# Performance work log

Hardware: AMD Instinct MI355X
Metric: run time of the kernel (lower is better)

Reference implementation:

```python
import jax, jax.numpy as jnp
import numpy as np

DIM = 1024
D_SRC = 1024
H = 16
HD = DIM // H
SCALE = 1.0 / np.sqrt(DIM)  # module uses 1/sqrt(internal_dim), not head_dim


def setup_inputs() -> dict:
    key = jax.random.key(0)
    ks = jax.random.split(key, 7)
    B, T = 2, 2048
    Q = jax.random.normal(ks[0], (B, T, DIM), dtype=jnp.float32)
    K = jax.random.normal(ks[1], (B, T, D_SRC), dtype=jnp.float32)
    V = jax.random.normal(ks[2], (B, T, D_SRC), dtype=jnp.float32)
    # torch nn.Linear weights: (out_features, in_features); y = x @ W.T
    s = 0.02
    Wq = jax.random.normal(ks[3], (DIM, DIM), dtype=jnp.float32) * s
    Wk = jax.random.normal(ks[4], (DIM, D_SRC), dtype=jnp.float32) * s
    Wv = jax.random.normal(ks[5], (DIM, D_SRC), dtype=jnp.float32) * s
    Wo = jax.random.normal(ks[6], (DIM, DIM), dtype=jnp.float32) * s
    return {"Q": Q, "K": K, "V": V, "Wq": Wq, "Wk": Wk, "Wv": Wv, "Wo": Wo}


def _split_heads(x):  # (B,T,DIM) -> (B,H,T,HD)
    B, T, _ = x.shape
    return x.reshape(B, T, H, HD).transpose(0, 2, 1, 3)


def reference(Q, K, V, Wq, Wk, Wv, Wo):
    B, T, _ = Q.shape
    q = _split_heads(Q @ Wq.T)
    k = _split_heads(K @ Wk.T)
    v = _split_heads(V @ Wv.T)
    att = jnp.einsum('bhid,bhjd->bhij', q, k) * SCALE
    causal = jnp.tril(jnp.ones((T, T), dtype=bool))
    att = jnp.where(causal[None, None], att, -jnp.inf)
    att = jax.nn.softmax(att, axis=-1)
    y = jnp.einsum('bhij,bhjd->bhid', att, v)
    y = y.transpose(0, 2, 1, 3).reshape(B, T, DIM)
    y = y @ Wo.T
    return y, att
```

## Files before the change

### kernel.cpp

```cpp
#include <hip/hip_runtime.h>
#include <hip/hip_bf16.h>

#define Bb 2
#define Tt 2048
#define DIMd 1024
#define Hh 16
#define HDh 64
#define MTOK (Bb * Tt)
#define NSCALE 0.03125f

typedef __attribute__((ext_vector_type(8))) short bf16x8;
typedef __attribute__((ext_vector_type(4))) float floatx4;

__device__ __forceinline__ unsigned short f2bf(float f) {
    union { float f; unsigned int u; } a; a.f = f;
    const unsigned int u = a.u;
    return (unsigned short)((u + 0x7FFFu + ((u >> 16) & 1u)) >> 16);
}

__device__ __forceinline__ bf16x8 cvt8(const float4 a, const float4 b) {
    bf16x8 r;
    r[0] = (short)f2bf(a.x); r[1] = (short)f2bf(a.y);
    r[2] = (short)f2bf(a.z); r[3] = (short)f2bf(a.w);
    r[4] = (short)f2bf(b.x); r[5] = (short)f2bf(b.y);
    r[6] = (short)f2bf(b.z); r[7] = (short)f2bf(b.w);
    return r;
}

__device__ __forceinline__ void gl_lds16(const void* g, void* l) {
    __builtin_amdgcn_global_load_lds((const __attribute__((address_space(1))) void*)g,
                                     (__attribute__((address_space(3))) void*)l, 16, 0, 0);
}

__global__ __launch_bounds__(256) void f32_to_bf16(const float* __restrict__ src,
                                                   unsigned short* __restrict__ dst, int n) {
    const int i = (blockIdx.x * 256 + threadIdx.x) * 4;
    if (i < n) {
        const float4 v = *(const float4*)(src + i);
        ushort4 o;
        o.x = f2bf(v.x); o.y = f2bf(v.y); o.z = f2bf(v.z); o.w = f2bf(v.w);
        *(ushort4*)(dst + i) = o;
    }
}

__global__ __launch_bounds__(256) void gemm_bt_mfma(const unsigned short* __restrict__ A,
                                                    const unsigned short* __restrict__ W,
                                                    float* __restrict__ C,
                                                    int M, int N, int K) {
    __shared__ unsigned short As[128 * 32];
    __shared__ unsigned short Bs[128 * 32];

    const int tid  = threadIdx.x;
    const int wave = tid >> 6;
    const int lane = tid & 63;
    const int m0 = blockIdx.y * 128;
    const int n0 = blockIdx.x * 128;
    const int wm = (wave >> 1) * 64;
    const int wn = (wave & 1) * 64;
    const int qd = lane >> 4;
    const int ln16 = lane & 15;

    floatx4 acc[4][4];
#pragma unroll
    for (int mi = 0; mi < 4; ++mi)
#pragma unroll
        for (int ni = 0; ni < 4; ++ni) acc[mi][ni] = (floatx4){0.f, 0.f, 0.f, 0.f};

    for (int k0 = 0; k0 < K; k0 += 32) {
#pragma unroll
        for (int t = 0; t < 2; ++t) {
            const int c = t * 256 + wave * 64 + lane;
            const int row = c >> 2;
            const int col = (c & 3) * 8;
            gl_lds16(A + (size_t)(m0 + row) * K + k0 + col, &As[c * 8]);
            gl_lds16(W + (size_t)(n0 + row) * K + k0 + col, &Bs[c * 8]);
        }
        __syncthreads();

        bf16x8 af[4], bfr[4];
#pragma unroll
        for (int mi = 0; mi < 4; ++mi)
            af[mi] = *(const bf16x8*)&As[(wm + mi * 16 + ln16) * 32 + qd * 8];
#pragma unroll
        for (int ni = 0; ni < 4; ++ni)
            bfr[ni] = *(const bf16x8*)&Bs[(wn + ni * 16 + ln16) * 32 + qd * 8];
#pragma unroll
        for (int mi = 0; mi < 4; ++mi)
#pragma unroll
            for (int ni = 0; ni < 4; ++ni)
                acc[mi][ni] = __builtin_amdgcn_mfma_f32_16x16x32_bf16(af[mi], bfr[ni], acc[mi][ni], 0, 0, 0);
        __syncthreads();
    }

#pragma unroll
    for (int mi = 0; mi < 4; ++mi)
#pragma unroll
        for (int ni = 0; ni < 4; ++ni) {
            const int gn = n0 + wn + ni * 16 + ln16;
#pragma unroll
            for (int r = 0; r < 4; ++r) {
                const int gm = m0 + wm + mi * 16 + qd * 4 + r;
                C[(size_t)gm * N + gn] = acc[mi][ni][r];
            }
        }
}

#define PSTR 72

__global__ __launch_bounds__(256) void fused_attn(const float* __restrict__ qp,
                                                  const float* __restrict__ kp,
                                                  const float* __restrict__ vt,
                                                  float* __restrict__ att,
                                                  unsigned short* __restrict__ ymid,
                                                  float* __restrict__ lws) {
    __shared__ unsigned short Ks[64 * PSTR];
    __shared__ unsigned short Vs[64 * PSTR];
    __shared__ unsigned short Ps[64 * PSTR];
    __shared__ float ls[64];

    const int bid = blockIdx.x;
    const int bh  = bid & 31;
    const int it  = 31 - (bid >> 5);
    const int h   = bh & (Hh - 1);
    const int b   = bh >> 4;
    const int tid = threadIdx.x;
    const int w    = tid >> 6;
    const int lane = tid & 63;
    const int qd   = lane >> 4;
    const int ln16 = lane & 15;
    const int i0   = it * 64;

    if (tid < 64) ls[tid] = 0.f;

    bf16x8 qf[2];
    {
        const float* qrow = qp + (size_t)(b * Tt + i0 + w * 16 + ln16) * DIMd + h * HDh;
#pragma unroll
        for (int ks = 0; ks < 2; ++ks) {
            const float4 a = *(const float4*)(qrow + ks * 32 + qd * 8);
            const float4 c = *(const float4*)(qrow + ks * 32 + qd * 8 + 4);
            qf[ks] = cvt8(a, c);
        }
    }

    const int srow = tid >> 2;
    const int scol = (tid & 3) * 16;

    floatx4 oacc[4];
#pragma unroll
    for (int dt = 0; dt < 4; ++dt) oacc[dt] = (floatx4){0.f, 0.f, 0.f, 0.f};

    unsigned short* Pw = &Ps[w * 16 * PSTR];
    const int qrow0 = w * 16 + qd * 4;

    for (int jt = 0; jt <= it; ++jt) {
        const int j0 = jt * 64;
        __syncthreads();

        {
            const float* kr = kp + (size_t)(b * Tt + j0 + srow) * DIMd + h * HDh + scol;
            const float4 k0 = ((const float4*)kr)[0];
            const float4 k1 = ((const float4*)kr)[1];
            const float4 k2 = ((const float4*)kr)[2];
            const float4 k3 = ((const float4*)kr)[3];
            *(bf16x8*)&Ks[srow * PSTR + scol]     = cvt8(k0, k1);
            *(bf16x8*)&Ks[srow * PSTR + scol + 8] = cvt8(k2, k3);
            const float* vr = vt + (size_t)(h * HDh + srow) * MTOK + b * Tt + j0 + scol;
            const float4 v0 = ((const float4*)vr)[0];
            const float4 v1 = ((const float4*)vr)[1];
            const float4 v2 = ((const float4*)vr)[2];
            const float4 v3 = ((const float4*)vr)[3];
            *(bf16x8*)&Vs[srow * PSTR + scol]     = cvt8(v0, v1);
            *(bf16x8*)&Vs[srow * PSTR + scol + 8] = cvt8(v2, v3);
        }
        __syncthreads();

        floatx4 sacc[4];
#pragma unroll
        for (int ct = 0; ct < 4; ++ct) sacc[ct] = (floatx4){0.f, 0.f, 0.f, 0.f};
#pragma unroll
        for (int ks = 0; ks < 2; ++ks)
#pragma unroll
            for (int ct = 0; ct < 4; ++ct) {
                const bf16x8 kf = *(const bf16x8*)&Ks[(ct * 16 + ln16) * PSTR + ks * 32 + qd * 8];
                sacc[ct] = __builtin_amdgcn_mfma_f32_16x16x32_bf16(qf[ks], kf, sacc[ct], 0, 0, 0);
            }

        float rs[4] = {0.f, 0.f, 0.f, 0.f};
#pragma unroll
        for (int r = 0; r < 4; ++r) {
            const int ig = i0 + qrow0 + r;
            float* arow = att + (size_t)(bh * Tt + ig) * Tt + j0;
            unsigned short* prow = &Pw[(qd * 4 + r) * PSTR];
#pragma unroll
            for (int ct = 0; ct < 4; ++ct) {
                const int jc = ct * 16 + ln16;
                const float e = (j0 + jc <= ig) ? __expf(sacc[ct][r] * NSCALE) : 0.f;
                arow[jc] = e;
                prow[jc] = f2bf(e);
                rs[r] += e;
            }
        }
#pragma unroll
        for (int r = 0; r < 4; ++r) {
            float v = rs[r];
            v += __shfl_xor(v, 1); v += __shfl_xor(v, 2);
            v += __shfl_xor(v, 4); v += __shfl_xor(v, 8);
            if (ln16 == 0) ls[qrow0 + r] += v;
        }

#pragma unroll
        for (int ks = 0; ks < 2; ++ks) {
            const bf16x8 pf = *(const bf16x8*)&Pw[ln16 * PSTR + ks * 32 + qd * 8];
#pragma unroll
            for (int dt = 0; dt < 4; ++dt) {
                const bf16x8 vf = *(const bf16x8*)&Vs[(dt * 16 + ln16) * PSTR + ks * 32 + qd * 8];
                oacc[dt] = __builtin_amdgcn_mfma_f32_16x16x32_bf16(pf, vf, oacc[dt], 0, 0, 0);
            }
        }
    }

#pragma unroll
    for (int r = 0; r < 4; ++r) {
        const float inv = 1.f / ls[qrow0 + r];
        unsigned short* yr = ymid + (size_t)(b * Tt + i0 + qrow0 + r) * DIMd + h * HDh + ln16;
#pragma unroll
        for (int dt = 0; dt < 4; ++dt)
            yr[dt * 16] = f2bf(oacc[dt][r] * inv);
    }
    if (tid < 64) lws[bh * Tt + i0 + tid] = ls[tid];
}

__global__ __launch_bounds__(256) void att_rescale(float* __restrict__ att,
                                                   const float* __restrict__ lws) {
    const int row = blockIdx.x;
    const int i   = row & (Tt - 1);
    const float inv = 1.f / lws[row];
    float4* arow = (float4*)(att + (size_t)row * Tt);
    const int tid = threadIdx.x;
#pragma unroll
    for (int q = 0; q < 2; ++q) {
        const int f4 = tid + q * 256;
        const int j  = f4 * 4;
        float4 v;
        if (j <= i) {
            v = arow[f4];
            v.x = (j + 0 <= i) ? v.x * inv : 0.f;
            v.y = (j + 1 <= i) ? v.y * inv : 0.f;
            v.z = (j + 2 <= i) ? v.z * inv : 0.f;
            v.w = (j + 3 <= i) ? v.w * inv : 0.f;
        } else {
            v = make_float4(0.f, 0.f, 0.f, 0.f);
        }
        arow[f4] = v;
    }
}

extern "C" void kernel_launch(void* const* d_in, const int* in_sizes, int n_in,
                              void* d_out, int out_size, void* d_ws, size_t ws_size,
                              hipStream_t stream) {
    const float* Q  = (const float*)d_in[0];
    const float* K  = (const float*)d_in[1];
    const float* V  = (const float*)d_in[2];
    const float* Wq = (const float*)d_in[3];
    const float* Wk = (const float*)d_in[4];
    const float* Wv = (const float*)d_in[5];
    const float* Wo = (const float*)d_in[6];

    const size_t nytok = (size_t)Bb * Tt * DIMd;
    const size_t nw    = (size_t)DIMd * DIMd;
    float* y   = (float*)d_out;
    float* att = y + nytok;

    char* w = (char*)d_ws;
    float* qp = (float*)w;                       w += nytok * 4;
    float* kp = (float*)w;                       w += nytok * 4;
    float* vt = (float*)w;                       w += nytok * 4;
    unsigned short* Qb  = (unsigned short*)w;    w += nytok * 2;
    unsigned short* Kb  = (unsigned short*)w;    w += nytok * 2;
    unsigned short* Vb  = (unsigned short*)w;    w += nytok * 2;
    unsigned short* Wqb = (unsigned short*)w;    w += nw * 2;
    unsigned short* Wkb = (unsigned short*)w;    w += nw * 2;
    unsigned short* Wvb = (unsigned short*)w;    w += nw * 2;
    unsigned short* Wob = (unsigned short*)w;    w += nw * 2;
    float* lws = (float*)w;
    unsigned short* ymid_b = Qb;

    const int M = Bb * Tt;

    f32_to_bf16<<<(int)(nytok / 1024), 256, 0, stream>>>(Q, Qb, (int)nytok);
    f32_to_bf16<<<(int)(nytok / 1024), 256, 0, stream>>>(K, Kb, (int)nytok);
    f32_to_bf16<<<(int)(nytok / 1024), 256, 0, stream>>>(V, Vb, (int)nytok);
    f32_to_bf16<<<(int)(nw / 1024), 256, 0, stream>>>(Wq, Wqb, (int)nw);
    f32_to_bf16<<<(int)(nw / 1024), 256, 0, stream>>>(Wk, Wkb, (int)nw);
    f32_to_bf16<<<(int)(nw / 1024), 256, 0, stream>>>(Wv, Wvb, (int)nw);
    f32_to_bf16<<<(int)(nw / 1024), 256, 0, stream>>>(Wo, Wob, (int)nw);

    dim3 gg(DIMd / 128, M / 128);
    gemm_bt_mfma<<<gg, 256, 0, stream>>>(Qb, Wqb, qp, M, DIMd, DIMd);
    gemm_bt_mfma<<<gg, 256, 0, stream>>>(Kb, Wkb, kp, M, DIMd, DIMd);
    dim3 ggv(M / 128, DIMd / 128);
    gemm_bt_mfma<<<ggv, 256, 0, stream>>>(Wvb, Vb, vt, DIMd, M, DIMd);

    fused_attn<<<32 * 32, 256, 0, stream>>>(qp, kp, vt, att, ymid_b, lws);
    att_rescale<<<Bb * Hh * Tt, 256, 0, stream>>>(att, lws);

    gemm_bt_mfma<<<gg, 256, 0, stream>>>(ymid_b, Wob, y, M, DIMd, DIMd);
}
```

Baseline: 866.1 us.

## Emit bf16 projections, fuse conversions, swizzle LDS and transpose score MFMA in attention

```diff
diff --git a/kernel.cpp b/kernel.cpp
--- a/kernel.cpp
+++ b/kernel.cpp
@@ -18,34 +18,42 @@
     return (unsigned short)((u + 0x7FFFu + ((u >> 16) & 1u)) >> 16);
 }
 
-__device__ __forceinline__ bf16x8 cvt8(const float4 a, const float4 b) {
-    bf16x8 r;
-    r[0] = (short)f2bf(a.x); r[1] = (short)f2bf(a.y);
-    r[2] = (short)f2bf(a.z); r[3] = (short)f2bf(a.w);
-    r[4] = (short)f2bf(b.x); r[5] = (short)f2bf(b.y);
-    r[6] = (short)f2bf(b.z); r[7] = (short)f2bf(b.w);
-    return r;
-}
-
 __device__ __forceinline__ void gl_lds16(const void* g, void* l) {
     __builtin_amdgcn_global_load_lds((const __attribute__((address_space(1))) void*)g,
                                      (__attribute__((address_space(3))) void*)l, 16, 0, 0);
 }
 
-__global__ __launch_bounds__(256) void f32_to_bf16(const float* __restrict__ src,
-                                                   unsigned short* __restrict__ dst, int n) {
-    const int i = (blockIdx.x * 256 + threadIdx.x) * 4;
-    if (i < n) {
-        const float4 v = *(const float4*)(src + i);
-        ushort4 o;
-        o.x = f2bf(v.x); o.y = f2bf(v.y); o.z = f2bf(v.z); o.w = f2bf(v.w);
-        *(ushort4*)(dst + i) = o;
-    }
-}
-
+__global__ __launch_bounds__(256) void cvt_all(
+    const float* __restrict__ s0, const float* __restrict__ s1, const float* __restrict__ s2,
+    const float* __restrict__ s3, const float* __restrict__ s4, const float* __restrict__ s5,
+    const float* __restrict__ s6,
+    unsigned short* __restrict__ d0, unsigned short* __restrict__ d1, unsigned short* __restrict__ d2,
+    unsigned short* __restrict__ d3, unsigned short* __restrict__ d4, unsigned short* __restrict__ d5,
+    unsigned short* __restrict__ d6) {
+    const int blk = blockIdx.x;
+    const float* src; unsigned short* dst; int rb;
+    if (blk < 12288) {
+        const int r = blk >> 12;
+        rb  = blk & 4095;
+        src = (r == 0) ? s0 : ((r == 1) ? s1 : s2);
+        dst = (r == 0) ? d0 : ((r == 1) ? d1 : d2);
+    } else {
+        const int r = (blk - 12288) >> 10;
+        rb  = blk & 1023;
+        src = (r == 0) ? s3 : ((r == 1) ? s4 : ((r == 2) ? s5 : s6));
+        dst = (r == 0) ? d3 : ((r == 1) ? d4 : ((r == 2) ? d5 : d6));
+    }
+    const int i = (rb * 256 + threadIdx.x) * 4;
+    const float4 v = *(const float4*)(src + i);
+    ushort4 o;
+    o.x = f2bf(v.x); o.y = f2bf(v.y); o.z = f2bf(v.z); o.w = f2bf(v.w);
+    *(ushort4*)(dst + i) = o;
+}
+
+template <int BF16OUT>
 __global__ __launch_bounds__(256) void gemm_bt_mfma(const unsigned short* __restrict__ A,
                                                     const unsigned short* __restrict__ W,
-                                                    float* __restrict__ C,
+                                                    void* __restrict__ Cv,
                                                     int M, int N, int K) {
     __shared__ unsigned short As[128 * 32];
     __shared__ unsigned short Bs[128 * 32];
@@ -100,135 +108,131 @@
 #pragma unroll
             for (int r = 0; r < 4; ++r) {
                 const int gm = m0 + wm + mi * 16 + qd * 4 + r;
-                C[(size_t)gm * N + gn] = acc[mi][ni][r];
+                if (BF16OUT)
+                    ((unsigned short*)Cv)[(size_t)gm * N + gn] = f2bf(acc[mi][ni][r]);
+                else
+                    ((float*)Cv)[(size_t)gm * N + gn] = acc[mi][ni][r];
             }
         }
 }
 
 #define PSTR 72
 
-__global__ __launch_bounds__(256) void fused_attn(const float* __restrict__ qp,
-                                                  const float* __restrict__ kp,
-                                                  const float* __restrict__ vt,
+__global__ __launch_bounds__(256) void fused_attn(const unsigned short* __restrict__ qp,
+                                                  const unsigned short* __restrict__ kp,
+                                                  const unsigned short* __restrict__ vt,
                                                   float* __restrict__ att,
                                                   unsigned short* __restrict__ ymid,
                                                   float* __restrict__ lws) {
-    __shared__ unsigned short Ks[64 * PSTR];
-    __shared__ unsigned short Vs[64 * PSTR];
+    __shared__ unsigned short Ks[64 * 64];
+    __shared__ unsigned short Vs[64 * 64];
     __shared__ unsigned short Ps[64 * PSTR];
-    __shared__ float ls[64];
 
     const int bid = blockIdx.x;
     const int bh  = bid & 31;
     const int it  = 31 - (bid >> 5);
     const int h   = bh & (Hh - 1);
     const int b   = bh >> 4;
-    const int tid = threadIdx.x;
+    const int tid  = threadIdx.x;
     const int w    = tid >> 6;
     const int lane = tid & 63;
     const int qd   = lane >> 4;
     const int ln16 = lane & 15;
     const int i0   = it * 64;
-
-    if (tid < 64) ls[tid] = 0.f;
+    const int ig   = i0 + w * 16 + ln16;
 
     bf16x8 qf[2];
     {
-        const float* qrow = qp + (size_t)(b * Tt + i0 + w * 16 + ln16) * DIMd + h * HDh;
-#pragma unroll
-        for (int ks = 0; ks < 2; ++ks) {
-            const float4 a = *(const float4*)(qrow + ks * 32 + qd * 8);
-            const float4 c = *(const float4*)(qrow + ks * 32 + qd * 8 + 4);
-            qf[ks] = cvt8(a, c);
-        }
-    }
-
-    const int srow = tid >> 2;
-    const int scol = (tid & 3) * 16;
+        const unsigned short* qrow = qp + (size_t)(b * Tt + ig) * DIMd + h * HDh;
+        qf[0] = *(const bf16x8*)(qrow + qd * 8);
+        qf[1] = *(const bf16x8*)(qrow + 32 + qd * 8);
+    }
 
     floatx4 oacc[4];
 #pragma unroll
     for (int dt = 0; dt < 4; ++dt) oacc[dt] = (floatx4){0.f, 0.f, 0.f, 0.f};
+    float lsum = 0.f;
 
     unsigned short* Pw = &Ps[w * 16 * PSTR];
-    const int qrow0 = w * 16 + qd * 4;
+    float* arow = att + ((size_t)bh * Tt + ig) * Tt;
 
     for (int jt = 0; jt <= it; ++jt) {
         const int j0 = jt * 64;
         __syncthreads();
 
-        {
-            const float* kr = kp + (size_t)(b * Tt + j0 + srow) * DIMd + h * HDh + scol;
-            const float4 k0 = ((const float4*)kr)[0];
-            const float4 k1 = ((const float4*)kr)[1];
-            const float4 k2 = ((const float4*)kr)[2];
-            const float4 k3 = ((const float4*)kr)[3];
-            *(bf16x8*)&Ks[srow * PSTR + scol]     = cvt8(k0, k1);
-            *(bf16x8*)&Ks[srow * PSTR + scol + 8] = cvt8(k2, k3);
-            const float* vr = vt + (size_t)(h * HDh + srow) * MTOK + b * Tt + j0 + scol;
-            const float4 v0 = ((const float4*)vr)[0];
-            const float4 v1 = ((const float4*)vr)[1];
-            const float4 v2 = ((const float4*)vr)[2];
-            const float4 v3 = ((const float4*)vr)[3];
-            *(bf16x8*)&Vs[srow * PSTR + scol]     = cvt8(v0, v1);
-            *(bf16x8*)&Vs[srow * PSTR + scol + 8] = cvt8(v2, v3);
+#pragma unroll
+        for (int t = 0; t < 2; ++t) {
+            const int c   = w * 128 + t * 64 + lane;
+            const int row = c >> 3;
+            const int cb  = c & 7;
+            const int col8 = ((cb ^ (row & 7)) * 8);
+            gl_lds16(kp + (size_t)(b * Tt + j0 + row) * DIMd + h * HDh + col8, &Ks[c * 8]);
+            gl_lds16(vt + (size_t)(h * HDh + row) * MTOK + b * Tt + j0 + col8, &Vs[c * 8]);
         }
         __syncthreads();
 
         floatx4 sacc[4];
 #pragma unroll
         for (int ct = 0; ct < 4; ++ct) sacc[ct] = (floatx4){0.f, 0.f, 0.f, 0.f};
+        __builtin_amdgcn_s_setprio(1);
 #pragma unroll
         for (int ks = 0; ks < 2; ++ks)
 #pragma unroll
             for (int ct = 0; ct < 4; ++ct) {
-                const bf16x8 kf = *(const bf16x8*)&Ks[(ct * 16 + ln16) * PSTR + ks * 32 + qd * 8];
-                sacc[ct] = __builtin_amdgcn_mfma_f32_16x16x32_bf16(qf[ks], kf, sacc[ct], 0, 0, 0);
+                const int row = ct * 16 + ln16;
+                const bf16x8 kf = *(const bf16x8*)&Ks[row * 64 + (((ks * 4 + qd) ^ (row & 7)) * 8)];
+                sacc[ct] = __builtin_amdgcn_mfma_f32_16x16x32_bf16(kf, qf[ks], sacc[ct], 0, 0, 0);
             }
-
-        float rs[4] = {0.f, 0.f, 0.f, 0.f};
-#pragma unroll
-        for (int r = 0; r < 4; ++r) {
-            const int ig = i0 + qrow0 + r;
-            float* arow = att + (size_t)(bh * Tt + ig) * Tt + j0;
-            unsigned short* prow = &Pw[(qd * 4 + r) * PSTR];
-#pragma unroll
-            for (int ct = 0; ct < 4; ++ct) {
-                const int jc = ct * 16 + ln16;
-                const float e = (j0 + jc <= ig) ? __expf(sacc[ct][r] * NSCALE) : 0.f;
-                arow[jc] = e;
-                prow[jc] = f2bf(e);
-                rs[r] += e;
+        __builtin_amdgcn_s_setprio(0);
+
+        float rs = 0.f;
+#pragma unroll
+        for (int ct = 0; ct < 4; ++ct) {
+            const int jb = j0 + ct * 16 + qd * 4;
+            float4 ev;
+            {
+                const float e0 = (jb + 0 <= ig) ? __expf(sacc[ct][0] * NSCALE) : 0.f;
+                const float e1 = (jb + 1 <= ig) ? __expf(sacc[ct][1] * NSCALE) : 0.f;
+                const float e2 = (jb + 2 <= ig) ? __expf(sacc[ct][2] * NSCALE) : 0.f;
+                const float e3 = (jb + 3 <= ig) ? __expf(sacc[ct][3] * NSCALE) : 0.f;
+                ev = make_float4(e0, e1, e2, e3);
+                rs += e0 + e1 + e2 + e3;
             }
-        }
-#pragma unroll
-        for (int r = 0; r < 4; ++r) {
-            float v = rs[r];
-            v += __shfl_xor(v, 1); v += __shfl_xor(v, 2);
-            v += __shfl_xor(v, 4); v += __shfl_xor(v, 8);
-            if (ln16 == 0) ls[qrow0 + r] += v;
-        }
-
+            *(float4*)(arow + jb) = ev;
+            ushort4 pk;
+            pk.x = f2bf(ev.x); pk.y = f2bf(ev.y); pk.z = f2bf(ev.z); pk.w = f2bf(ev.w);
+            *(ushort4*)&Pw[ln16 * PSTR + ct * 16 + qd * 4] = pk;
+        }
+        rs += __shfl_xor(rs, 16);
+        rs += __shfl_xor(rs, 32);
+        lsum += rs;
+
+        __builtin_amdgcn_s_setprio(1);
 #pragma unroll
         for (int ks = 0; ks < 2; ++ks) {
             const bf16x8 pf = *(const bf16x8*)&Pw[ln16 * PSTR + ks * 32 + qd * 8];
 #pragma unroll
             for (int dt = 0; dt < 4; ++dt) {
-                const bf16x8 vf = *(const bf16x8*)&Vs[(dt * 16 + ln16) * PSTR + ks * 32 + qd * 8];
+                const int row = dt * 16 + ln16;
+                const bf16x8 vf = *(const bf16x8*)&Vs[row * 64 + (((ks * 4 + qd) ^ (row & 7)) * 8)];
                 oacc[dt] = __builtin_amdgcn_mfma_f32_16x16x32_bf16(pf, vf, oacc[dt], 0, 0, 0);
             }
         }
-    }
-
+        __builtin_amdgcn_s_setprio(0);
+    }
+
+    float lssrc[4];
+#pragma unroll
+    for (int r = 0; r < 4; ++r) lssrc[r] = __shfl(lsum, qd * 4 + r);
 #pragma unroll
     for (int r = 0; r < 4; ++r) {
-        const float inv = 1.f / ls[qrow0 + r];
-        unsigned short* yr = ymid + (size_t)(b * Tt + i0 + qrow0 + r) * DIMd + h * HDh + ln16;
+        const float inv = 1.f / lssrc[r];
+        unsigned short* yr = ymid + (size_t)(b * Tt + i0 + w * 16 + qd * 4 + r) * DIMd + h * HDh + ln16;
 #pragma unroll
         for (int dt = 0; dt < 4; ++dt)
             yr[dt * 16] = f2bf(oacc[dt][r] * inv);
     }
-    if (tid < 64) lws[bh * Tt + i0 + tid] = ls[tid];
+    if (qd == 0) lws[(size_t)bh * Tt + ig] = lsum;
 }
 
 __global__ __launch_bounds__(256) void att_rescale(float* __restrict__ att,
@@ -273,9 +277,9 @@
     float* att = y + nytok;
 
     char* w = (char*)d_ws;
-    float* qp = (float*)w;                       w += nytok * 4;
-    float* kp = (float*)w;                       w += nytok * 4;
-    float* vt = (float*)w;                       w += nytok * 4;
+    unsigned short* qp  = (unsigned short*)w;    w += nytok * 2;
+    unsigned short* kp  = (unsigned short*)w;    w += nytok * 2;
+    unsigned short* vt  = (unsigned short*)w;    w += nytok * 2;
     unsigned short* Qb  = (unsigned short*)w;    w += nytok * 2;
     unsigned short* Kb  = (unsigned short*)w;    w += nytok * 2;
     unsigned short* Vb  = (unsigned short*)w;    w += nytok * 2;
@@ -288,22 +292,17 @@
 
     const int M = Bb * Tt;
 
-    f32_to_bf16<<<(int)(nytok / 1024), 256, 0, stream>>>(Q, Qb, (int)nytok);
-    f32_to_bf16<<<(int)(nytok / 1024), 256, 0, stream>>>(K, Kb, (int)nytok);
-    f32_to_bf16<<<(int)(nytok / 1024), 256, 0, stream>>>(V, Vb, (int)nytok);
-    f32_to_bf16<<<(int)(nw / 1024), 256, 0, stream>>>(Wq, Wqb, (int)nw);
-    f32_to_bf16<<<(int)(nw / 1024), 256, 0, stream>>>(Wk, Wkb, (int)nw);
-    f32_to_bf16<<<(int)(nw / 1024), 256, 0, stream>>>(Wv, Wvb, (int)nw);
-    f32_to_bf16<<<(int)(nw / 1024), 256, 0, stream>>>(Wo, Wob, (int)nw);
+    cvt_all<<<16384, 256, 0, stream>>>(Q, K, V, Wq, Wk, Wv, Wo,
+                                       Qb, Kb, Vb, Wqb, Wkb, Wvb, Wob);
 
     dim3 gg(DIMd / 128, M / 128);
-    gemm_bt_mfma<<<gg, 256, 0, stream>>>(Qb, Wqb, qp, M, DIMd, DIMd);
-    gemm_bt_mfma<<<gg, 256, 0, stream>>>(Kb, Wkb, kp, M, DIMd, DIMd);
+    gemm_bt_mfma<1><<<gg, 256, 0, stream>>>(Qb, Wqb, qp, M, DIMd, DIMd);
+    gemm_bt_mfma<1><<<gg, 256, 0, stream>>>(Kb, Wkb, kp, M, DIMd, DIMd);
     dim3 ggv(M / 128, DIMd / 128);
-    gemm_bt_mfma<<<ggv, 256, 0, stream>>>(Wvb, Vb, vt, DIMd, M, DIMd);
+    gemm_bt_mfma<1><<<ggv, 256, 0, stream>>>(Wvb, Vb, vt, DIMd, M, DIMd);
 
     fused_attn<<<32 * 32, 256, 0, stream>>>(qp, kp, vt, att, ymid_b, lws);
     att_rescale<<<Bb * Hh * Tt, 256, 0, stream>>>(att, lws);
 
-    gemm_bt_mfma<<<gg, 256, 0, stream>>>(ymid_b, Wob, y, M, DIMd, DIMd);
-}
+    gemm_bt_mfma<0><<<gg, 256, 0, stream>>>(ymid_b, Wob, y, M, DIMd, DIMd);
+}
```

New measurement: 830.6 us. 1.04x faster.
